# Kernel optimization log

Measured on AMD Instinct MI355X. Metric: run time of the kernel, lower is better.

Reference implementation:

```python
import jax, jax.numpy as jnp
import numpy as np

H = 32  # hidden_size hardcoded in CHIVE
T, B = 2048, 2048
D_F, D_P, D_S = 8, 8, 24


def setup_inputs() -> dict:
    key = jax.random.key(0)
    ks = jax.random.split(key, 16)
    s = 0.1  # weight scale
    return {
        "frnn_seq": jax.random.normal(ks[0], (T, B, D_F), jnp.float32),
        "phrnn_seq": jax.random.normal(ks[1], (T, B, D_P), jnp.float32),
        "sylrnn_seq": jax.random.normal(ks[2], (T, B, D_S), jnp.float32),
        "Wx_f": jax.random.normal(ks[3], (D_F, H), jnp.float32) * s,
        "Wh_f": jax.random.normal(ks[4], (H, H), jnp.float32) * s,
        "b_f": jnp.zeros((H,), jnp.float32),
        "Wx_p": jax.random.normal(ks[5], (D_P, H), jnp.float32) * s,
        "Wh_p": jax.random.normal(ks[6], (H, H), jnp.float32) * s,
        "b_p": jnp.zeros((H,), jnp.float32),
        "Wx_s": jax.random.normal(ks[7], (H, H), jnp.float32) * s,
        "Wh_s": jax.random.normal(ks[8], (H, H), jnp.float32) * s,
        "b_s": jnp.zeros((H,), jnp.float32),
        "frnn_clock": jax.random.randint(ks[9], (T,), 0, 8, jnp.int32),
        "phrnn_clock": jax.random.randint(ks[10], (T,), 0, 8, jnp.int32),
        "sample_freq": jax.random.randint(ks[11], (T,), 0, 2, jnp.int32),
    }


def reference(frnn_seq, phrnn_seq, sylrnn_seq,
              Wx_f, Wh_f, b_f, Wx_p, Wh_p, b_p, Wx_s, Wh_s, b_s,
              frnn_clock, phrnn_clock, sample_freq):
    # Clockwork cell: update h only when timestep % clock_val == 0.
    # Clocks are offset +1 so the modulus is always >= 1.
    t_idx = jnp.arange(T)
    upd_f = (t_idx % (frnn_clock + 1)) == 0          # [T] bool
    upd_p = (t_idx % (phrnn_clock + 1)) == 0
    # the syl layer updates exactly when sample_freq[t] == 1.
    upd_s = sample_freq == 1

    # Static pad of syl input to max_length = max(H, H, D_S) = H (D_S <= H).
    syl_padded = jnp.pad(sylrnn_seq, ((0, 0), (0, 0), (0, H - D_S)))  # [T,B,H]

    def cell(x, h, Wx, Wh, b, upd):
        h_new = jnp.tanh(x @ Wx + h @ Wh + b)
        return jnp.where(upd, h_new, h)

    def step(carry, inputs):
        h_f, h_p, h_s = carry
        x_f, x_p, x_s, uf, up, us = inputs
        h_f = cell(x_f, h_f, Wx_f, Wh_f, b_f, uf)        # [B,H]
        h_p = cell(x_p, h_p, Wx_p, Wh_p, b_p, up)        # [B,H]
        x_stack = jnp.stack([h_f, h_p, x_s], axis=0)     # [3,B,H]
        h_s = cell(x_stack, h_s, Wx_s, Wh_s, b_s, us)    # [3,B,H]
        return (h_f, h_p, h_s), None

    h0 = jnp.zeros((B, H), frnn_seq.dtype)
    h0s = jnp.zeros((3, B, H), frnn_seq.dtype)
    (h_f, h_p, h_s), _ = jax.lax.scan(
        step, (h0, h0, h0s),
        (frnn_seq, phrnn_seq, syl_padded, upd_f, upd_p, upd_s))
    return h_s
```

## Files before the change

### kernel.cpp

```cpp
#include <hip/hip_runtime.h>


constexpr int TS  = 2048;
constexpr int B   = 2048;
constexpr int HH  = 32;
constexpr int CH  = 16;
constexpr int NCH = TS / CH;
constexpr int BPB = 8;

__device__ __forceinline__ float fast_tanh(float x) {
    x = fminf(fmaxf(x, -9.0f), 9.0f);
    float e = __expf(2.0f * x);
    return (e - 1.0f) * __builtin_amdgcn_rcpf(e + 1.0f);
}

__global__ __launch_bounds__(256, 1)
void chive_rnn(const float* __restrict__ frnn, const float* __restrict__ phrnn,
               const float* __restrict__ syl,
               const float* __restrict__ Wxf, const float* __restrict__ Whf,
               const float* __restrict__ bf,
               const float* __restrict__ Wxp, const float* __restrict__ Whp,
               const float* __restrict__ bp,
               const float* __restrict__ Wxs, const float* __restrict__ Whs,
               const float* __restrict__ bs,
               const int* __restrict__ fclock, const int* __restrict__ pclock,
               const int* __restrict__ sfreq, float* __restrict__ out)
{
    __shared__ __align__(16) float xfb[2][CH][BPB * 8];
    __shared__ __align__(16) float xpb[2][CH][BPB * 8];
    __shared__ __align__(16) float xsb[2][CH][BPB * 24];
    __shared__ __align__(16) float hf[BPB][HH];
    __shared__ __align__(16) float hp[BPB][HH];
    __shared__ __align__(16) float hs[3][BPB][HH];
    __shared__ int gates[TS];

    const int tid = threadIdx.x;
    const int j   = tid & 31;
    const int g   = tid >> 5;
    const int b0  = blockIdx.x * BPB;

    float wxf[8], whf_r[32], wxp[8], whp_r[32], wxs_r[32], whs_r[32];
#pragma unroll
    for (int i = 0; i < 8;  i++) wxf[i]   = Wxf[i * HH + j];
#pragma unroll
    for (int i = 0; i < 32; i++) whf_r[i] = Whf[i * HH + j];
#pragma unroll
    for (int i = 0; i < 8;  i++) wxp[i]   = Wxp[i * HH + j];
#pragma unroll
    for (int i = 0; i < 32; i++) whp_r[i] = Whp[i * HH + j];
#pragma unroll
    for (int i = 0; i < 32; i++) wxs_r[i] = Wxs[i * HH + j];
#pragma unroll
    for (int i = 0; i < 32; i++) whs_r[i] = Whs[i * HH + j];
    const float bfj = bf[j], bpj = bp[j], bsj = bs[j];

    float4 rf, rp, rs0, rs1, rs2;
    const int tl = tid >> 4;
    const int q  = tid & 15;

    auto load_chunk = [&](int ch) {
        const size_t t  = (size_t)ch * CH + tl;
        const float* fb = frnn  + (t * B + b0) * 8;
        const float* pb = phrnn + (t * B + b0) * 8;
        const float* sb = syl   + (t * B + b0) * 24;
        rf  = *(const float4*)(fb + q * 4);
        rp  = *(const float4*)(pb + q * 4);
        rs0 = *(const float4*)(sb + q * 4);
        rs1 = *(const float4*)(sb + 64 + q * 4);
        rs2 = *(const float4*)(sb + 128 + q * 4);
    };
    auto store_chunk = [&](int buf) {
        *(float4*)&xfb[buf][tl][q * 4]       = rf;
        *(float4*)&xpb[buf][tl][q * 4]       = rp;
        *(float4*)&xsb[buf][tl][q * 4]       = rs0;
        *(float4*)&xsb[buf][tl][64 + q * 4]  = rs1;
        *(float4*)&xsb[buf][tl][128 + q * 4] = rs2;
    };

    load_chunk(0);

    for (int i = tid; i < TS; i += 256) {
        int mf = fclock[i] + 1;
        int mp = pclock[i] + 1;
        int v = 0;
        if ((i % mf) == 0)  v |= 1;
        if ((i % mp) == 0)  v |= 2;
        if (sfreq[i] == 1)  v |= 4;
        gates[i] = v;
    }

    hf[g][j] = 0.f; hp[g][j] = 0.f;
    hs[0][g][j] = 0.f; hs[1][g][j] = 0.f; hs[2][g][j] = 0.f;

    store_chunk(0);
    __syncthreads();

    int cur = 0;
#pragma unroll 1
    for (int ch = 0; ch < NCH; ch++) {
        if (ch + 1 < NCH) load_chunk(ch + 1);

#pragma unroll 1
        for (int c = 0; c < CH; c++) {
            const int t  = ch * CH + c;
            const int gt = __builtin_amdgcn_readfirstlane(gates[t]);

            if (gt & 1) {
                float4 a = {bfj, 0.f, 0.f, 0.f};
                const float4* xv = (const float4*)&xfb[cur][c][g * 8];
                float4 x0 = xv[0], x1 = xv[1];
                a.x = fmaf(x0.x, wxf[0], a.x); a.y = fmaf(x0.y, wxf[1], a.y);
                a.z = fmaf(x0.z, wxf[2], a.z); a.w = fmaf(x0.w, wxf[3], a.w);
                a.x = fmaf(x1.x, wxf[4], a.x); a.y = fmaf(x1.y, wxf[5], a.y);
                a.z = fmaf(x1.z, wxf[6], a.z); a.w = fmaf(x1.w, wxf[7], a.w);
#pragma unroll
                for (int kk = 0; kk < 8; kk++) {
                    float4 h4 = *(const float4*)&hf[g][kk * 4];
                    a.x = fmaf(h4.x, whf_r[kk*4+0], a.x);
                    a.y = fmaf(h4.y, whf_r[kk*4+1], a.y);
                    a.z = fmaf(h4.z, whf_r[kk*4+2], a.z);
                    a.w = fmaf(h4.w, whf_r[kk*4+3], a.w);
                }
                hf[g][j] = fast_tanh((a.x + a.y) + (a.z + a.w));
            }

            if (gt & 2) {
                float4 a = {bpj, 0.f, 0.f, 0.f};
                const float4* xv = (const float4*)&xpb[cur][c][g * 8];
                float4 x0 = xv[0], x1 = xv[1];
                a.x = fmaf(x0.x, wxp[0], a.x); a.y = fmaf(x0.y, wxp[1], a.y);
                a.z = fmaf(x0.z, wxp[2], a.z); a.w = fmaf(x0.w, wxp[3], a.w);
                a.x = fmaf(x1.x, wxp[4], a.x); a.y = fmaf(x1.y, wxp[5], a.y);
                a.z = fmaf(x1.z, wxp[6], a.z); a.w = fmaf(x1.w, wxp[7], a.w);
#pragma unroll
                for (int kk = 0; kk < 8; kk++) {
                    float4 h4 = *(const float4*)&hp[g][kk * 4];
                    a.x = fmaf(h4.x, whp_r[kk*4+0], a.x);
                    a.y = fmaf(h4.y, whp_r[kk*4+1], a.y);
                    a.z = fmaf(h4.z, whp_r[kk*4+2], a.z);
                    a.w = fmaf(h4.w, whp_r[kk*4+3], a.w);
                }
                hp[g][j] = fast_tanh((a.x + a.y) + (a.z + a.w));
            }

            if (gt & 4) {
                float4 a0 = {bsj, 0.f, 0.f, 0.f};
                float4 a1 = {bsj, 0.f, 0.f, 0.f};
                float4 a2 = {bsj, 0.f, 0.f, 0.f};
#pragma unroll
                for (int kk = 0; kk < 8; kk++) {
                    float4 hf4 = *(const float4*)&hf[g][kk * 4];
                    float4 hp4 = *(const float4*)&hp[g][kk * 4];
                    float w0 = wxs_r[kk*4+0], w1 = wxs_r[kk*4+1];
                    float w2 = wxs_r[kk*4+2], w3 = wxs_r[kk*4+3];
                    a0.x = fmaf(hf4.x, w0, a0.x); a0.y = fmaf(hf4.y, w1, a0.y);
                    a0.z = fmaf(hf4.z, w2, a0.z); a0.w = fmaf(hf4.w, w3, a0.w);
                    a1.x = fmaf(hp4.x, w0, a1.x); a1.y = fmaf(hp4.y, w1, a1.y);
                    a1.z = fmaf(hp4.z, w2, a1.z); a1.w = fmaf(hp4.w, w3, a1.w);
                }
#pragma unroll
                for (int kk = 0; kk < 6; kk++) {
                    float4 x4 = *(const float4*)&xsb[cur][c][g * 24 + kk * 4];
                    a2.x = fmaf(x4.x, wxs_r[kk*4+0], a2.x);
                    a2.y = fmaf(x4.y, wxs_r[kk*4+1], a2.y);
                    a2.z = fmaf(x4.z, wxs_r[kk*4+2], a2.z);
                    a2.w = fmaf(x4.w, wxs_r[kk*4+3], a2.w);
                }
#pragma unroll
                for (int kk = 0; kk < 8; kk++) {
                    float4 h0 = *(const float4*)&hs[0][g][kk * 4];
                    float4 h1 = *(const float4*)&hs[1][g][kk * 4];
                    float4 h2 = *(const float4*)&hs[2][g][kk * 4];
                    float w0 = whs_r[kk*4+0], w1 = whs_r[kk*4+1];
                    float w2 = whs_r[kk*4+2], w3 = whs_r[kk*4+3];
                    a0.x = fmaf(h0.x, w0, a0.x); a0.y = fmaf(h0.y, w1, a0.y);
                    a0.z = fmaf(h0.z, w2, a0.z); a0.w = fmaf(h0.w, w3, a0.w);
                    a1.x = fmaf(h1.x, w0, a1.x); a1.y = fmaf(h1.y, w1, a1.y);
                    a1.z = fmaf(h1.z, w2, a1.z); a1.w = fmaf(h1.w, w3, a1.w);
                    a2.x = fmaf(h2.x, w0, a2.x); a2.y = fmaf(h2.y, w1, a2.y);
                    a2.z = fmaf(h2.z, w2, a2.z); a2.w = fmaf(h2.w, w3, a2.w);
                }
                hs[0][g][j] = fast_tanh((a0.x + a0.y) + (a0.z + a0.w));
                hs[1][g][j] = fast_tanh((a1.x + a1.y) + (a1.z + a1.w));
                hs[2][g][j] = fast_tanh((a2.x + a2.y) + (a2.z + a2.w));
            }
        }

        if (ch + 1 < NCH) store_chunk(cur ^ 1);
        __syncthreads();
        cur ^= 1;
    }

    const int b = b0 + g;
    out[((size_t)0 * B + b) * HH + j] = hs[0][g][j];
    out[((size_t)1 * B + b) * HH + j] = hs[1][g][j];
    out[((size_t)2 * B + b) * HH + j] = hs[2][g][j];
}

extern "C" void kernel_launch(void* const* d_in, const int* in_sizes, int n_in,
                              void* d_out, int out_size, void* d_ws, size_t ws_size,
                              hipStream_t stream) {
    const float* frnn  = (const float*)d_in[0];
    const float* phrnn = (const float*)d_in[1];
    const float* syl   = (const float*)d_in[2];
    const float* Wxf   = (const float*)d_in[3];
    const float* Whf   = (const float*)d_in[4];
    const float* bf    = (const float*)d_in[5];
    const float* Wxp   = (const float*)d_in[6];
    const float* Whp   = (const float*)d_in[7];
    const float* bp    = (const float*)d_in[8];
    const float* Wxs   = (const float*)d_in[9];
    const float* Whs   = (const float*)d_in[10];
    const float* bs    = (const float*)d_in[11];
    const int* fclock  = (const int*)d_in[12];
    const int* pclock  = (const int*)d_in[13];
    const int* sfreq   = (const int*)d_in[14];
    float* out = (float*)d_out;

    dim3 grid(B / BPB);
    dim3 block(256);
    chive_rnn<<<grid, block, 0, stream>>>(frnn, phrnn, syl,
                                          Wxf, Whf, bf, Wxp, Whp, bp,
                                          Wxs, Whs, bs,
                                          fclock, pclock, sfreq, out);
}
```

Measured before the change: 1.666 ms.

## Keep hidden states in registers and compute matvecs with DPP lane rotations

Hidden states move out of LDS into per-lane registers, and each 32x32 recurrent matvec is computed with DPP row rotations plus a 16-lane swizzle, using weights pre-permuted to match the rotation order. The syl input buffer is padded to 32 columns so each lane reads its own element. The Wxs projections of hf and hp are cached and recomputed only when those states change. This removes LDS round-trips on the serial recurrence path, at the cost of cross-lane rotation latency and more complex weight indexing.

```diff
diff --git a/kernel.cpp b/kernel.cpp
--- a/kernel.cpp
+++ b/kernel.cpp
@@ -13,6 +13,29 @@
     float e = __expf(2.0f * x);
     return (e - 1.0f) * __builtin_amdgcn_rcpf(e + 1.0f);
 }
+
+__device__ __forceinline__ float rotr1(float x) {
+    int i = __float_as_int(x);
+    i = __builtin_amdgcn_update_dpp(i, i, 0x121, 0xF, 0xF, false);
+    return __int_as_float(i);
+}
+
+__device__ __forceinline__ float swap16(float x) {
+    return __int_as_float(__builtin_amdgcn_ds_swizzle(__float_as_int(x), 0x401F));
+}
+
+#define GDOT32(res, hval, W) do {                                   \
+    float _ra = (hval);                                             \
+    float _rb = swap16(_ra);                                        \
+    float _aA = 0.f, _aB = 0.f;                                     \
+    _Pragma("unroll")                                               \
+    for (int _s = 0; _s < 16; _s++) {                               \
+        _aA = fmaf(_ra, W[_s], _aA);                                \
+        _aB = fmaf(_rb, W[16 + _s], _aB);                           \
+        if (_s < 15) { _ra = rotr1(_ra); _rb = rotr1(_rb); }        \
+    }                                                               \
+    (res) = _aA + _aB;                                              \
+} while (0)
 
 __global__ __launch_bounds__(256, 1)
 void chive_rnn(const float* __restrict__ frnn, const float* __restrict__ phrnn,
@@ -28,35 +51,41 @@
 {
     __shared__ __align__(16) float xfb[2][CH][BPB * 8];
     __shared__ __align__(16) float xpb[2][CH][BPB * 8];
-    __shared__ __align__(16) float xsb[2][CH][BPB * 24];
-    __shared__ __align__(16) float hf[BPB][HH];
-    __shared__ __align__(16) float hp[BPB][HH];
-    __shared__ __align__(16) float hs[3][BPB][HH];
+    __shared__ __align__(16) float xsb[2][CH][BPB * 32];
     __shared__ int gates[TS];
 
     const int tid = threadIdx.x;
     const int j   = tid & 31;
     const int g   = tid >> 5;
     const int b0  = blockIdx.x * BPB;
-
-    float wxf[8], whf_r[32], wxp[8], whp_r[32], wxs_r[32], whs_r[32];
+    const int p   = j & 15;
+    const int R   = j >> 4;
+
+    int pr = __builtin_amdgcn_update_dpp(p, p, 0x121, 0xF, 0xF, false);
+    const int dir = (pr == ((p - 1) & 15)) ? 1 : -1;
+
+    float whf_r[32], whp_r[32], wxs_r[32], whs_r[32];
 #pragma unroll
-    for (int i = 0; i < 8;  i++) wxf[i]   = Wxf[i * HH + j];
+    for (int s = 0; s < 32; s++) {
+        int Re = (s < 16) ? R : 1 - R;
+        int k  = Re * 16 + ((p - dir * s) & 15);
+        whf_r[s] = Whf[k * HH + j];
+        whp_r[s] = Whp[k * HH + j];
+        wxs_r[s] = Wxs[k * HH + j];
+        whs_r[s] = Whs[k * HH + j];
+    }
+    float wxf[8], wxp[8];
 #pragma unroll
-    for (int i = 0; i < 32; i++) whf_r[i] = Whf[i * HH + j];
-#pragma unroll
-    for (int i = 0; i < 8;  i++) wxp[i]   = Wxp[i * HH + j];
-#pragma unroll
-    for (int i = 0; i < 32; i++) whp_r[i] = Whp[i * HH + j];
-#pragma unroll
-    for (int i = 0; i < 32; i++) wxs_r[i] = Wxs[i * HH + j];
-#pragma unroll
-    for (int i = 0; i < 32; i++) whs_r[i] = Whs[i * HH + j];
+    for (int i = 0; i < 8; i++) { wxf[i] = Wxf[i * HH + j]; wxp[i] = Wxp[i * HH + j]; }
     const float bfj = bf[j], bpj = bp[j], bsj = bs[j];
 
     float4 rf, rp, rs0, rs1, rs2;
     const int tl = tid >> 4;
     const int q  = tid & 15;
+    const int ss0 = q * 4, ss1 = 64 + q * 4, ss2 = 128 + q * 4;
+    const int d0 = (ss0 / 24) * 32 + (ss0 % 24);
+    const int d1 = (ss1 / 24) * 32 + (ss1 % 24);
+    const int d2 = (ss2 / 24) * 32 + (ss2 % 24);
 
     auto load_chunk = [&](int ch) {
         const size_t t  = (size_t)ch * CH + tl;
@@ -65,19 +94,26 @@
         const float* sb = syl   + (t * B + b0) * 24;
         rf  = *(const float4*)(fb + q * 4);
         rp  = *(const float4*)(pb + q * 4);
-        rs0 = *(const float4*)(sb + q * 4);
-        rs1 = *(const float4*)(sb + 64 + q * 4);
-        rs2 = *(const float4*)(sb + 128 + q * 4);
+        rs0 = *(const float4*)(sb + ss0);
+        rs1 = *(const float4*)(sb + ss1);
+        rs2 = *(const float4*)(sb + ss2);
     };
     auto store_chunk = [&](int buf) {
-        *(float4*)&xfb[buf][tl][q * 4]       = rf;
-        *(float4*)&xpb[buf][tl][q * 4]       = rp;
-        *(float4*)&xsb[buf][tl][q * 4]       = rs0;
-        *(float4*)&xsb[buf][tl][64 + q * 4]  = rs1;
-        *(float4*)&xsb[buf][tl][128 + q * 4] = rs2;
+        *(float4*)&xfb[buf][tl][q * 4] = rf;
+        *(float4*)&xpb[buf][tl][q * 4] = rp;
+        *(float4*)&xsb[buf][tl][d0]    = rs0;
+        *(float4*)&xsb[buf][tl][d1]    = rs1;
+        *(float4*)&xsb[buf][tl][d2]    = rs2;
     };
 
     load_chunk(0);
+
+    {
+        const int bb = tid >> 7, rr = (tid >> 3) & 15, cc = tid & 7;
+        float4 z = {0.f, 0.f, 0.f, 0.f};
+        *(float4*)&xsb[bb][rr][cc * 32 + 24] = z;
+        *(float4*)&xsb[bb][rr][cc * 32 + 28] = z;
+    }
 
     for (int i = tid; i < TS; i += 256) {
         int mf = fclock[i] + 1;
@@ -89,8 +125,9 @@
         gates[i] = v;
     }
 
-    hf[g][j] = 0.f; hp[g][j] = 0.f;
-    hs[0][g][j] = 0.f; hs[1][g][j] = 0.f; hs[2][g][j] = 0.f;
+    float hfv = 0.f, hpv = 0.f, hs0 = 0.f, hs1 = 0.f, hs2 = 0.f;
+    float s0x = 0.f, s1x = 0.f;
+    bool fdirty = false, pdirty = false;
 
     store_chunk(0);
     __syncthreads();
@@ -106,83 +143,42 @@
             const int gt = __builtin_amdgcn_readfirstlane(gates[t]);
 
             if (gt & 1) {
-                float4 a = {bfj, 0.f, 0.f, 0.f};
                 const float4* xv = (const float4*)&xfb[cur][c][g * 8];
                 float4 x0 = xv[0], x1 = xv[1];
-                a.x = fmaf(x0.x, wxf[0], a.x); a.y = fmaf(x0.y, wxf[1], a.y);
-                a.z = fmaf(x0.z, wxf[2], a.z); a.w = fmaf(x0.w, wxf[3], a.w);
-                a.x = fmaf(x1.x, wxf[4], a.x); a.y = fmaf(x1.y, wxf[5], a.y);
-                a.z = fmaf(x1.z, wxf[6], a.z); a.w = fmaf(x1.w, wxf[7], a.w);
-#pragma unroll
-                for (int kk = 0; kk < 8; kk++) {
-                    float4 h4 = *(const float4*)&hf[g][kk * 4];
-                    a.x = fmaf(h4.x, whf_r[kk*4+0], a.x);
-                    a.y = fmaf(h4.y, whf_r[kk*4+1], a.y);
-                    a.z = fmaf(h4.z, whf_r[kk*4+2], a.z);
-                    a.w = fmaf(h4.w, whf_r[kk*4+3], a.w);
-                }
-                hf[g][j] = fast_tanh((a.x + a.y) + (a.z + a.w));
+                float a = bfj;
+                a = fmaf(x0.x, wxf[0], a); a = fmaf(x0.y, wxf[1], a);
+                a = fmaf(x0.z, wxf[2], a); a = fmaf(x0.w, wxf[3], a);
+                a = fmaf(x1.x, wxf[4], a); a = fmaf(x1.y, wxf[5], a);
+                a = fmaf(x1.z, wxf[6], a); a = fmaf(x1.w, wxf[7], a);
+                float hh; GDOT32(hh, hfv, whf_r);
+                hfv = fast_tanh(a + hh);
+                fdirty = true;
             }
 
             if (gt & 2) {
-                float4 a = {bpj, 0.f, 0.f, 0.f};
                 const float4* xv = (const float4*)&xpb[cur][c][g * 8];
                 float4 x0 = xv[0], x1 = xv[1];
-                a.x = fmaf(x0.x, wxp[0], a.x); a.y = fmaf(x0.y, wxp[1], a.y);
-                a.z = fmaf(x0.z, wxp[2], a.z); a.w = fmaf(x0.w, wxp[3], a.w);
-                a.x = fmaf(x1.x, wxp[4], a.x); a.y = fmaf(x1.y, wxp[5], a.y);
-                a.z = fmaf(x1.z, wxp[6], a.z); a.w = fmaf(x1.w, wxp[7], a.w);
-#pragma unroll
-                for (int kk = 0; kk < 8; kk++) {
-                    float4 h4 = *(const float4*)&hp[g][kk * 4];
-                    a.x = fmaf(h4.x, whp_r[kk*4+0], a.x);
-                    a.y = fmaf(h4.y, whp_r[kk*4+1], a.y);
-                    a.z = fmaf(h4.z, whp_r[kk*4+2], a.z);
-                    a.w = fmaf(h4.w, whp_r[kk*4+3], a.w);
-                }
-                hp[g][j] = fast_tanh((a.x + a.y) + (a.z + a.w));
+                float a = bpj;
+                a = fmaf(x0.x, wxp[0], a); a = fmaf(x0.y, wxp[1], a);
+                a = fmaf(x0.z, wxp[2], a); a = fmaf(x0.w, wxp[3], a);
+                a = fmaf(x1.x, wxp[4], a); a = fmaf(x1.y, wxp[5], a);
+                a = fmaf(x1.z, wxp[6], a); a = fmaf(x1.w, wxp[7], a);
+                float hh; GDOT32(hh, hpv, whp_r);
+                hpv = fast_tanh(a + hh);
+                pdirty = true;
             }
 
             if (gt & 4) {
-                float4 a0 = {bsj, 0.f, 0.f, 0.f};
-                float4 a1 = {bsj, 0.f, 0.f, 0.f};
-                float4 a2 = {bsj, 0.f, 0.f, 0.f};
-#pragma unroll
-                for (int kk = 0; kk < 8; kk++) {
-                    float4 hf4 = *(const float4*)&hf[g][kk * 4];
-                    float4 hp4 = *(const float4*)&hp[g][kk * 4];
-                    float w0 = wxs_r[kk*4+0], w1 = wxs_r[kk*4+1];
-                    float w2 = wxs_r[kk*4+2], w3 = wxs_r[kk*4+3];
-                    a0.x = fmaf(hf4.x, w0, a0.x); a0.y = fmaf(hf4.y, w1, a0.y);
-                    a0.z = fmaf(hf4.z, w2, a0.z); a0.w = fmaf(hf4.w, w3, a0.w);
-                    a1.x = fmaf(hp4.x, w0, a1.x); a1.y = fmaf(hp4.y, w1, a1.y);
-                    a1.z = fmaf(hp4.z, w2, a1.z); a1.w = fmaf(hp4.w, w3, a1.w);
-                }
-#pragma unroll
-                for (int kk = 0; kk < 6; kk++) {
-                    float4 x4 = *(const float4*)&xsb[cur][c][g * 24 + kk * 4];
-                    a2.x = fmaf(x4.x, wxs_r[kk*4+0], a2.x);
-                    a2.y = fmaf(x4.y, wxs_r[kk*4+1], a2.y);
-                    a2.z = fmaf(x4.z, wxs_r[kk*4+2], a2.z);
-                    a2.w = fmaf(x4.w, wxs_r[kk*4+3], a2.w);
-                }
-#pragma unroll
-                for (int kk = 0; kk < 8; kk++) {
-                    float4 h0 = *(const float4*)&hs[0][g][kk * 4];
-                    float4 h1 = *(const float4*)&hs[1][g][kk * 4];
-                    float4 h2 = *(const float4*)&hs[2][g][kk * 4];
-                    float w0 = whs_r[kk*4+0], w1 = whs_r[kk*4+1];
-                    float w2 = whs_r[kk*4+2], w3 = whs_r[kk*4+3];
-                    a0.x = fmaf(h0.x, w0, a0.x); a0.y = fmaf(h0.y, w1, a0.y);
-                    a0.z = fmaf(h0.z, w2, a0.z); a0.w = fmaf(h0.w, w3, a0.w);
-                    a1.x = fmaf(h1.x, w0, a1.x); a1.y = fmaf(h1.y, w1, a1.y);
-                    a1.z = fmaf(h1.z, w2, a1.z); a1.w = fmaf(h1.w, w3, a1.w);
-                    a2.x = fmaf(h2.x, w0, a2.x); a2.y = fmaf(h2.y, w1, a2.y);
-                    a2.z = fmaf(h2.z, w2, a2.z); a2.w = fmaf(h2.w, w3, a2.w);
-                }
-                hs[0][g][j] = fast_tanh((a0.x + a0.y) + (a0.z + a0.w));
-                hs[1][g][j] = fast_tanh((a1.x + a1.y) + (a1.z + a1.w));
-                hs[2][g][j] = fast_tanh((a2.x + a2.y) + (a2.z + a2.w));
+                if (fdirty) { GDOT32(s0x, hfv, wxs_r); fdirty = false; }
+                if (pdirty) { GDOT32(s1x, hpv, wxs_r); pdirty = false; }
+                float xs = xsb[cur][c][g * 32 + j];
+                float s2x; GDOT32(s2x, xs,  wxs_r);
+                float m0;  GDOT32(m0,  hs0, whs_r);
+                float m1;  GDOT32(m1,  hs1, whs_r);
+                float m2;  GDOT32(m2,  hs2, whs_r);
+                hs0 = fast_tanh(bsj + s0x + m0);
+                hs1 = fast_tanh(bsj + s1x + m1);
+                hs2 = fast_tanh(bsj + s2x + m2);
             }
         }
 
@@ -192,9 +188,9 @@
     }
 
     const int b = b0 + g;
-    out[((size_t)0 * B + b) * HH + j] = hs[0][g][j];
-    out[((size_t)1 * B + b) * HH + j] = hs[1][g][j];
-    out[((size_t)2 * B + b) * HH + j] = hs[2][g][j];
+    out[((size_t)0 * B + b) * HH + j] = hs0;
+    out[((size_t)1 * B + b) * HH + j] = hs1;
+    out[((size_t)2 * B + b) * HH + j] = hs2;
 }
 
 extern "C" void kernel_launch(void* const* d_in, const int* in_sizes, int n_in,
```

Measured after the change: 1.770 ms. +6.3%, slower.
